# Kernel optimization log

Measured on AMD Instinct MI355X. Metric: run time of the kernel, lower is better.

## Reference

```python
import jax, jax.numpy as jnp
import numpy as np

EPS = 1e-5

def _bn_eval(x, gamma, beta, mean, var):
    return (x - mean) * (gamma / jnp.sqrt(var + EPS)) + beta

def setup_inputs() -> dict:
    key = jax.random.key(0)
    ks = jax.random.split(key, 12)
    N, E, D, C, H = 100000, 1000000, 64, 32, 128
    fused = 4 * D + C  # 288
    z = jax.random.normal(ks[0], (N, D), dtype=jnp.float32)
    edge_index = jax.random.randint(ks[1], (2, E), 0, N, dtype=jnp.int64)
    edge_context = jax.random.normal(ks[2], (E, C), dtype=jnp.float32)
    W1 = jax.random.normal(ks[3], (fused, H), dtype=jnp.float32) / np.sqrt(fused)
    b1 = jnp.zeros((H,), jnp.float32)
    g1 = jnp.ones((H,), jnp.float32); be1 = jnp.zeros((H,), jnp.float32)
    m1 = jnp.zeros((H,), jnp.float32); v1 = jnp.ones((H,), jnp.float32)
    W2 = jax.random.normal(ks[4], (H, H // 2), dtype=jnp.float32) / np.sqrt(H)
    b2 = jnp.zeros((H // 2,), jnp.float32)
    g2 = jnp.ones((H // 2,), jnp.float32); be2 = jnp.zeros((H // 2,), jnp.float32)
    m2 = jnp.zeros((H // 2,), jnp.float32); v2 = jnp.ones((H // 2,), jnp.float32)
    W3 = jax.random.normal(ks[5], (H // 2, 1), dtype=jnp.float32) / np.sqrt(H // 2)
    b3 = jnp.zeros((1,), jnp.float32)
    return {"z": z, "edge_index": edge_index, "edge_context": edge_context,
            "W1": W1, "b1": b1, "g1": g1, "be1": be1, "m1": m1, "v1": v1,
            "W2": W2, "b2": b2, "g2": g2, "be2": be2, "m2": m2, "v2": v2,
            "W3": W3, "b3": b3}

def reference(z, edge_index, edge_context,
              W1, b1, g1, be1, m1, v1,
              W2, b2, g2, be2, m2, v2,
              W3, b3):
    # gather endpoint embeddings: [E, D]
    src = z[edge_index[0]]
    dst = z[edge_index[1]]
    # fused features: [E, 4*D + C]
    fused = jnp.concatenate([src, dst, src * dst, jnp.abs(src - dst), edge_context], axis=1)
    x = jax.nn.relu(_bn_eval(fused @ W1 + b1, g1, be1, m1, v1))
    x = jax.nn.relu(_bn_eval(x @ W2 + b2, g2, be2, m2, v2))
    return (x @ W3 + b3).reshape(-1)
```

## Files before the change

kernel.cpp:

```cpp
#include <hip/hip_runtime.h>
#include <hip/hip_bf16.h>

typedef __attribute__((ext_vector_type(8))) short bf16x8;
typedef __attribute__((ext_vector_type(4))) float f32x4;
typedef __attribute__((ext_vector_type(4))) unsigned int u32x4;
typedef __attribute__((ext_vector_type(2))) unsigned int u32x2;
typedef __attribute__((ext_vector_type(2))) __bf16 bf16x2v;

#define EPS 1e-5f

__device__ inline unsigned short f2bf(float x) {
  unsigned int u = __builtin_bit_cast(unsigned int, x);
  unsigned int r = (u + 0x7FFFu + ((u >> 16) & 1u)) >> 16;
  return (unsigned short)r;
}

__device__ inline unsigned int cvtpk(float a, float b) {
  bf16x2v v = {(__bf16)a, (__bf16)b};
  return __builtin_bit_cast(unsigned int, v);
}

#define MFMA16(A, B, C) __builtin_amdgcn_mfma_f32_16x16x32_bf16((A), (B), (C), 0, 0, 0)

__global__ void prep_kernel(const float* __restrict__ W1, const float* __restrict__ W2,
                            const float* __restrict__ b1, const float* __restrict__ g1,
                            const float* __restrict__ be1, const float* __restrict__ m1,
                            const float* __restrict__ v1,
                            const float* __restrict__ b2, const float* __restrict__ g2,
                            const float* __restrict__ be2, const float* __restrict__ m2,
                            const float* __restrict__ v2,
                            unsigned short* __restrict__ w1f, unsigned short* __restrict__ w2f,
                            float* __restrict__ sc) {
  int t = blockIdx.x * 256 + threadIdx.x;
  if (t < 36864) {
    int j = t & 7, l = (t >> 3) & 63, f = t >> 9;
    int kb = f >> 3, nb = f & 7;
    int rk = kb * 32 + ((l >> 4) << 3) + j;
    int cn = (nb << 4) + (l & 15);
    w1f[t] = f2bf(W1[rk * 128 + cn]);
  } else if (t < 45056) {
    int o = t - 36864;
    int j = o & 7, l = (o >> 3) & 63, f = o >> 9;
    int kb = f >> 2, nb = f & 3;
    int s = kb * 32 + ((l >> 4) << 3) + j;
    int rk = (s & 96) | ((s & 1) << 4) | ((s >> 1) & 15);
    int cn = (nb << 4) + (l & 15);
    w2f[o] = f2bf(W2[rk * 64 + cn]);
  } else if (t < 45184) {
    int j = t - 45056;
    float s = g1[j] * rsqrtf(v1[j] + EPS);
    sc[j] = s;
    sc[128 + j] = (b1[j] - m1[j]) * s + be1[j];
  } else if (t < 45248) {
    int j = t - 45184;
    float s = g2[j] * rsqrtf(v2[j] + EPS);
    sc[256 + j] = s;
    sc[320 + j] = (b2[j] - m2[j]) * s + be2[j];
  }
}

#define F_SC_OFF 73728
#define F_A_OFF 75776
#define F_L3_OFF 157696
#define F_LDS_TOTAL 158720

#define WRITE_A_F()                                                                              \
  do {                                                                                           \
    const int rswz_ = (sr & 7) << 4;                                                             \
    char* rowp_ = AR + sr * 640;                                                                 \
    u32x4 ps_ = {cvtpk(sv0[0], sv0[1]), cvtpk(sv0[2], sv0[3]), cvtpk(sv1[0], sv1[1]),            \
                 cvtpk(sv1[2], sv1[3])};                                                         \
    u32x4 pd_ = {cvtpk(dv0[0], dv0[1]), cvtpk(dv0[2], dv0[3]), cvtpk(dv1[0], dv1[1]),            \
                 cvtpk(dv1[2], dv1[3])};                                                         \
    u32x4 pp_ = {cvtpk(sv0[0] * dv0[0], sv0[1] * dv0[1]), cvtpk(sv0[2] * dv0[2], sv0[3] * dv0[3]),\
                 cvtpk(sv1[0] * dv1[0], sv1[1] * dv1[1]), cvtpk(sv1[2] * dv1[2], sv1[3] * dv1[3])};\
    u32x4 pa_ = {cvtpk(fabsf(sv0[0] - dv0[0]), fabsf(sv0[1] - dv0[1])),                          \
                 cvtpk(fabsf(sv0[2] - dv0[2]), fabsf(sv0[3] - dv0[3])),                          \
                 cvtpk(fabsf(sv1[0] - dv1[0]), fabsf(sv1[1] - dv1[1])),                          \
                 cvtpk(fabsf(sv1[2] - dv1[2]), fabsf(sv1[3] - dv1[3]))};                         \
    u32x2 pc_ = {cvtpk(cv[0], cv[1]), cvtpk(cv[2], cv[3])};                                      \
    *(u32x4*)(rowp_ + ((sh * 16) ^ rswz_)) = ps_;                                                \
    *(u32x4*)(rowp_ + ((128 + sh * 16) ^ rswz_)) = pd_;                                          \
    *(u32x4*)(rowp_ + ((256 + sh * 16) ^ rswz_)) = pp_;                                          \
    *(u32x4*)(rowp_ + ((384 + sh * 16) ^ rswz_)) = pa_;                                          \
    *(u32x2*)(rowp_ + 512 + ((sh * 8) ^ rswz_)) = pc_;                                           \
  } while (0)

#define GATHER_NEXT_F(tg)                                                                        \
  do {                                                                                           \
    const f32x4* zs_ = (const f32x4*)(z + ((size_t)i0n * 64 + sh * 8));                          \
    sv0 = zs_[0];                                                                                \
    sv1 = zs_[1];                                                                                \
    const f32x4* zd_ = (const f32x4*)(z + ((size_t)i1n * 64 + sh * 8));                          \
    dv0 = zd_[0];                                                                                \
    dv1 = zd_[1];                                                                                \
    int eg_ = ((tg) << 7) + sr;                                                                  \
    int esg_ = eg_ < E ? eg_ : E - 1;                                                            \
    cv = *(const f32x4*)(ctx + (size_t)esg_ * 32 + sh * 4);                                      \
    int tn_ = (tg) + grid;                                                                       \
    if (tn_ >= nblk) tn_ = (tg);                                                                 \
    int en_ = (tn_ << 7) + sr;                                                                   \
    int esn_ = en_ < E ? en_ : E - 1;                                                            \
    i0n = ei[esn_];                                                                              \
    i1n = ei[E + esn_];                                                                          \
  } while (0)

__global__ __launch_bounds__(1024, 4) void fused_kernel_f(
    const float* __restrict__ z, const int* __restrict__ ei, const float* __restrict__ ctx,
    const unsigned short* __restrict__ w1f, const unsigned short* __restrict__ w2f,
    const float* __restrict__ sc, const float* __restrict__ w3, const float* __restrict__ b3,
    float* __restrict__ out, int E, int nblk) {
  extern __shared__ char lds[];
  char* W1L = lds;
  float* SC = (float*)(lds + F_SC_OFF);
  char* AR = lds + F_A_OFF;
  char* X1 = lds + F_A_OFF;
  float* l3 = (float*)(lds + F_L3_OFF);

  const int tid = threadIdx.x;
  const int lane = tid & 63, wave = tid >> 6;
  const int g = lane >> 4, lq = lane & 15;
  const int wr = wave >> 2, wc = wave & 3;
  const int w2r = wave >> 1, w2c = wave & 1;
  const int sr = tid >> 3, sh = tid & 7;
  const int grid = gridDim.x;

  {
    const f32x4* s = (const f32x4*)w1f;
    f32x4* d = (f32x4*)W1L;
#pragma unroll
    for (int i = 0; i < 4; i++) d[i * 1024 + tid] = s[i * 1024 + tid];
    if (tid < 512) d[4096 + tid] = s[4096 + tid];
    if (tid < 128) {
      SC[tid] = sc[tid];
      SC[128 + tid] = sc[128 + tid];
    } else if (tid < 192) {
      int j = tid - 128;
      SC[256 + j] = sc[256 + j];
      SC[320 + j] = sc[320 + j];
      SC[384 + j] = w3[j];
    } else if (tid == 192) {
      SC[448] = b3[0];
    }
  }

  bf16x8 w2g0, w2g1, w2g2, w2g3, w2h0, w2h1, w2h2, w2h3;
  {
    const bf16x8* W2G = (const bf16x8*)w2f;
    w2g0 = W2G[(0 * 4 + w2c * 2 + 0) * 64 + lane];
    w2h0 = W2G[(0 * 4 + w2c * 2 + 1) * 64 + lane];
    w2g1 = W2G[(1 * 4 + w2c * 2 + 0) * 64 + lane];
    w2h1 = W2G[(1 * 4 + w2c * 2 + 1) * 64 + lane];
    w2g2 = W2G[(2 * 4 + w2c * 2 + 0) * 64 + lane];
    w2h2 = W2G[(2 * 4 + w2c * 2 + 1) * 64 + lane];
    w2g3 = W2G[(3 * 4 + w2c * 2 + 0) * 64 + lane];
    w2h3 = W2G[(3 * 4 + w2c * 2 + 1) * 64 + lane];
  }

  f32x4 sv0, sv1, dv0, dv1, cv;
  int i0n, i1n;
  int t = blockIdx.x;

  {
    int e = (t << 7) + sr;
    int es = e < E ? e : E - 1;
    int a0 = ei[es], a1 = ei[E + es];
    cv = *(const f32x4*)(ctx + (size_t)es * 32 + sh * 4);
    const f32x4* zs = (const f32x4*)(z + ((size_t)a0 * 64 + sh * 8));
    sv0 = zs[0];
    sv1 = zs[1];
    const f32x4* zd = (const f32x4*)(z + ((size_t)a1 * 64 + sh * 8));
    dv0 = zd[0];
    dv1 = zd[1];
    int tn = t + grid;
    if (tn >= nblk) tn = t;
    int en = (tn << 7) + sr;
    int esn = en < E ? en : E - 1;
    i0n = ei[esn];
    i1n = ei[E + esn];
  }
  WRITE_A_F();
  {
    int tn = t + grid;
    if (tn >= nblk) tn = t;
    GATHER_NEXT_F(tn);
  }
  __syncthreads();

  for (; t < nblk; t += grid) {
    f32x4 acc00 = {0.f, 0.f, 0.f, 0.f}, acc01 = acc00, acc10 = acc00, acc11 = acc00;
    const bf16x8* W1F = (const bf16x8*)W1L;
    const int row0 = wr * 32 + lq, row1 = row0 + 16;
    const int swz0 = (row0 & 7) << 4, swz1 = (row1 & 7) << 4;
    const char* ap0 = AR + row0 * 640;
    const char* ap1 = AR + row1 * 640;
#pragma unroll
    for (int kb = 0; kb < 9; kb++) {
      bf16x8 a0 = *(const bf16x8*)(ap0 + ((kb * 64 + g * 16) ^ swz0));
      bf16x8 a1 = *(const bf16x8*)(ap1 + ((kb * 64 + g * 16) ^ swz1));
      bf16x8 b0 = W1F[(kb * 8 + wc * 2 + 0) * 64 + lane];
      bf16x8 b1 = W1F[(kb * 8 + wc * 2 + 1) * 64 + lane];
      acc00 = MFMA16(a0, b0, acc00);
      acc01 = MFMA16(a0, b1, acc01);
      acc10 = MFMA16(a1, b0, acc10);
      acc11 = MFMA16(a1, b1, acc11);
    }
    __syncthreads();

    {
      const int col0 = wc * 32 + lq;
      const float s1v0 = SC[col0], c1v0 = SC[128 + col0];
      const float s1v1 = SC[col0 + 16], c1v1 = SC[128 + col0 + 16];
      const int xoff = wc * 64 + lq * 4;
#pragma unroll
      for (int j = 0; j < 4; j++) {
        int rowa = wr * 32 + 4 * g + j;
        unsigned int pA = cvtpk(fmaxf(acc00[j] * s1v0 + c1v0, 0.f),
                                fmaxf(acc01[j] * s1v1 + c1v1, 0.f));
        *(unsigned int*)(X1 + rowa * 256 + (xoff ^ ((rowa & 7) << 4))) = pA;
        int rowb = rowa + 16;
        unsigned int pB = cvtpk(fmaxf(acc10[j] * s1v0 + c1v0, 0.f),
                                fmaxf(acc11[j] * s1v1 + c1v1, 0.f));
        *(unsigned int*)(X1 + rowb * 256 + (xoff ^ ((rowb & 7) << 4))) = pB;
      }
    }
    __syncthreads();

    f32x4 acc2A = {0.f, 0.f, 0.f, 0.f}, acc2B = acc2A;
    {
      const int row = w2r * 16 + lq;
      const int swz = (row & 7) << 4;
      const char* xp = X1 + row * 256;
      bf16x8 a0 = *(const bf16x8*)(xp + ((0 * 64 + g * 16) ^ swz));
      acc2A = MFMA16(a0, w2g0, acc2A);
      acc2B = MFMA16(a0, w2h0, acc2B);
      bf16x8 a1 = *(const bf16x8*)(xp + ((1 * 64 + g * 16) ^ swz));
      acc2A = MFMA16(a1, w2g1, acc2A);
      acc2B = MFMA16(a1, w2h1, acc2B);
      bf16x8 a2 = *(const bf16x8*)(xp + ((2 * 64 + g * 16) ^ swz));
      acc2A = MFMA16(a2, w2g2, acc2A);
      acc2B = MFMA16(a2, w2h2, acc2B);
      bf16x8 a3 = *(const bf16x8*)(xp + ((3 * 64 + g * 16) ^ swz));
      acc2A = MFMA16(a3, w2g3, acc2A);
      acc2B = MFMA16(a3, w2h3, acc2B);
    }

    const int colA = w2c * 32 + lq, colB = colA + 16;
    const float s2A = SC[256 + colA], c2A = SC[320 + colA];
    const float s2B = SC[256 + colB], c2B = SC[320 + colB];
    const float w3A = SC[384 + colA], w3B = SC[384 + colB];
#pragma unroll
    for (int j = 0; j < 4; j++) {
      float vA = fmaxf(acc2A[j] * s2A + c2A, 0.f);
      float vB = fmaxf(acc2B[j] * s2B + c2B, 0.f);
      float p = vA * w3A + vB * w3B;
      p += __shfl_xor(p, 1);
      p += __shfl_xor(p, 2);
      p += __shfl_xor(p, 4);
      p += __shfl_xor(p, 8);
      if (lq == 0) l3[(w2r * 16 + 4 * g + j) * 2 + w2c] = p;
    }
    __syncthreads();

    WRITE_A_F();
    {
      int tn2 = t + 2 * grid;
      if (tn2 >= nblk) tn2 = t + grid < nblk ? t + grid : t;
      GATHER_NEXT_F(tn2);
    }
    if (tid < 128) {
      int e = (t << 7) + tid;
      if (e < E) out[e] = l3[tid * 2] + l3[tid * 2 + 1] + SC[448];
    }
    __syncthreads();
  }
}

extern "C" void kernel_launch(void* const* d_in, const int* in_sizes, int n_in,
                              void* d_out, int out_size, void* d_ws, size_t ws_size,
                              hipStream_t stream) {
  const float* z = (const float*)d_in[0];
  const int* ei = (const int*)d_in[1];
  const float* ctx = (const float*)d_in[2];
  const float* W1 = (const float*)d_in[3];
  const float* b1 = (const float*)d_in[4];
  const float* g1 = (const float*)d_in[5];
  const float* be1 = (const float*)d_in[6];
  const float* m1 = (const float*)d_in[7];
  const float* v1 = (const float*)d_in[8];
  const float* W2 = (const float*)d_in[9];
  const float* b2 = (const float*)d_in[10];
  const float* g2 = (const float*)d_in[11];
  const float* be2 = (const float*)d_in[12];
  const float* m2 = (const float*)d_in[13];
  const float* v2 = (const float*)d_in[14];
  const float* W3 = (const float*)d_in[15];
  const float* b3 = (const float*)d_in[16];
  float* out = (float*)d_out;
  const int E = out_size;

  unsigned short* w1f = (unsigned short*)d_ws;
  unsigned short* w2f = (unsigned short*)((char*)d_ws + 73728);
  float* sc = (float*)((char*)d_ws + 90112);

  prep_kernel<<<177, 256, 0, stream>>>(W1, W2, b1, g1, be1, m1, v1,
                                       b2, g2, be2, m2, v2, w1f, w2f, sc);

  const int nblk = (E + 127) >> 7;
  (void)hipFuncSetAttribute((const void*)fused_kernel_f,
                            hipFuncAttributeMaxDynamicSharedMemorySize, F_LDS_TOTAL);
  fused_kernel_f<<<256, 1024, F_LDS_TOTAL, stream>>>(z, ei, ctx, w1f, w2f, sc, W3, b3,
                                                     out, E, nblk);
}
```

Before: 137.1 us.

## Derive product and abs-diff features from bf16 src/dst in registers instead of LDS

Adds a variant fused kernel whose LDS A tile holds only src, dst and context (384 bytes per row instead of 640). The src*dst and |src-dst| MFMA operands are recomputed in registers from the bf16 fragments already loaded for the src/dst MFMAs. This cuts LDS writes, reads and footprint but adds per-wave VALU work inside the layer-1 loop. The products are now formed from bf16-rounded inputs, which changes numerics slightly. The host falls back to the old kernel if the new one spills to scratch.

```diff
diff --git a/kernel.cpp b/kernel.cpp
--- a/kernel.cpp
+++ b/kernel.cpp
@@ -21,6 +21,23 @@
 }
 
 #define MFMA16(A, B, C) __builtin_amdgcn_mfma_f32_16x16x32_bf16((A), (B), (C), 0, 0, 0)
+
+__device__ inline void derive_pa(bf16x8 s, bf16x8 d, bf16x8* pr, bf16x8* ad) {
+  u32x4 su = __builtin_bit_cast(u32x4, s);
+  u32x4 du = __builtin_bit_cast(u32x4, d);
+  u32x4 pu, au;
+#pragma unroll
+  for (int i = 0; i < 4; i++) {
+    float slo = __builtin_bit_cast(float, su[i] << 16);
+    float shi = __builtin_bit_cast(float, su[i] & 0xFFFF0000u);
+    float dlo = __builtin_bit_cast(float, du[i] << 16);
+    float dhi = __builtin_bit_cast(float, du[i] & 0xFFFF0000u);
+    pu[i] = cvtpk(slo * dlo, shi * dhi);
+    au[i] = cvtpk(fabsf(slo - dlo), fabsf(shi - dhi));
+  }
+  *pr = __builtin_bit_cast(bf16x8, pu);
+  *ad = __builtin_bit_cast(bf16x8, au);
+}
 
 __global__ void prep_kernel(const float* __restrict__ W1, const float* __restrict__ W2,
                             const float* __restrict__ b1, const float* __restrict__ g1,
@@ -59,6 +76,243 @@
   }
 }
 
+#define V_SC_OFF 73728
+#define V_A_OFF 75776
+#define V_L3_OFF 124928
+#define V_LDS_TOTAL 125952
+
+#define WRITE_A_V()                                                                              \
+  do {                                                                                           \
+    const int rswz_ = (sr & 7) << 4;                                                             \
+    char* rowp_ = AV + sr * 384;                                                                 \
+    u32x4 ps_ = {cvtpk(sv0[0], sv0[1]), cvtpk(sv0[2], sv0[3]), cvtpk(sv1[0], sv1[1]),            \
+                 cvtpk(sv1[2], sv1[3])};                                                         \
+    u32x4 pd_ = {cvtpk(dv0[0], dv0[1]), cvtpk(dv0[2], dv0[3]), cvtpk(dv1[0], dv1[1]),            \
+                 cvtpk(dv1[2], dv1[3])};                                                         \
+    u32x2 pc_ = {cvtpk(cv[0], cv[1]), cvtpk(cv[2], cv[3])};                                      \
+    *(u32x4*)(rowp_ + ((sh * 16) ^ rswz_)) = ps_;                                                \
+    *(u32x4*)(rowp_ + ((128 + sh * 16) ^ rswz_)) = pd_;                                          \
+    *(u32x2*)(rowp_ + ((256 + sh * 8) ^ rswz_)) = pc_;                                           \
+  } while (0)
+
+#define GATHER_NEXT_V(tg)                                                                        \
+  do {                                                                                           \
+    const f32x4* zs_ = (const f32x4*)(z + ((size_t)i0n * 64 + sh * 8));                          \
+    sv0 = zs_[0];                                                                                \
+    sv1 = zs_[1];                                                                                \
+    const f32x4* zd_ = (const f32x4*)(z + ((size_t)i1n * 64 + sh * 8));                          \
+    dv0 = zd_[0];                                                                                \
+    dv1 = zd_[1];                                                                                \
+    int eg_ = ((tg) << 7) + sr;                                                                  \
+    int esg_ = eg_ < E ? eg_ : E - 1;                                                            \
+    cv = *(const f32x4*)(ctx + (size_t)esg_ * 32 + sh * 4);                                      \
+    int tn_ = (tg) + grid;                                                                       \
+    if (tn_ >= nblk) tn_ = (tg);                                                                 \
+    int en_ = (tn_ << 7) + sr;                                                                   \
+    int esn_ = en_ < E ? en_ : E - 1;                                                            \
+    i0n = ei[esn_];                                                                              \
+    i1n = ei[E + esn_];                                                                          \
+  } while (0)
+
+#define L1PAIR_V(KS)                                                                             \
+  do {                                                                                           \
+    bf16x8 s0_ = *(const bf16x8*)(ap0 + (((KS) * 64 + g * 16) ^ swz0));                          \
+    bf16x8 s1_ = *(const bf16x8*)(ap1 + (((KS) * 64 + g * 16) ^ swz0));                          \
+    bf16x8 d0_ = *(const bf16x8*)(ap0 + ((128 + (KS) * 64 + g * 16) ^ swz0));                    \
+    bf16x8 d1_ = *(const bf16x8*)(ap1 + ((128 + (KS) * 64 + g * 16) ^ swz0));                    \
+    bf16x8 b0_ = W1F[((KS) * 8 + wc * 2 + 0) * 64 + lane];                                       \
+    bf16x8 b1_ = W1F[((KS) * 8 + wc * 2 + 1) * 64 + lane];                                       \
+    acc00 = MFMA16(s0_, b0_, acc00); acc01 = MFMA16(s0_, b1_, acc01);                            \
+    acc10 = MFMA16(s1_, b0_, acc10); acc11 = MFMA16(s1_, b1_, acc11);                            \
+    b0_ = W1F[(((KS) + 2) * 8 + wc * 2 + 0) * 64 + lane];                                        \
+    b1_ = W1F[(((KS) + 2) * 8 + wc * 2 + 1) * 64 + lane];                                        \
+    acc00 = MFMA16(d0_, b0_, acc00); acc01 = MFMA16(d0_, b1_, acc01);                            \
+    acc10 = MFMA16(d1_, b0_, acc10); acc11 = MFMA16(d1_, b1_, acc11);                            \
+    bf16x8 p0_, a0_, p1_, a1_;                                                                   \
+    derive_pa(s0_, d0_, &p0_, &a0_);                                                             \
+    derive_pa(s1_, d1_, &p1_, &a1_);                                                             \
+    b0_ = W1F[(((KS) + 4) * 8 + wc * 2 + 0) * 64 + lane];                                        \
+    b1_ = W1F[(((KS) + 4) * 8 + wc * 2 + 1) * 64 + lane];                                        \
+    acc00 = MFMA16(p0_, b0_, acc00); acc01 = MFMA16(p0_, b1_, acc01);                            \
+    acc10 = MFMA16(p1_, b0_, acc10); acc11 = MFMA16(p1_, b1_, acc11);                            \
+    b0_ = W1F[(((KS) + 6) * 8 + wc * 2 + 0) * 64 + lane];                                        \
+    b1_ = W1F[(((KS) + 6) * 8 + wc * 2 + 1) * 64 + lane];                                        \
+    acc00 = MFMA16(a0_, b0_, acc00); acc01 = MFMA16(a0_, b1_, acc01);                            \
+    acc10 = MFMA16(a1_, b0_, acc10); acc11 = MFMA16(a1_, b1_, acc11);                            \
+  } while (0)
+
+__global__ __launch_bounds__(1024) void fused_kernel_v(
+    const float* __restrict__ z, const int* __restrict__ ei, const float* __restrict__ ctx,
+    const unsigned short* __restrict__ w1f, const unsigned short* __restrict__ w2f,
+    const float* __restrict__ sc, const float* __restrict__ w3, const float* __restrict__ b3,
+    float* __restrict__ out, int E, int nblk) {
+  extern __shared__ char lds[];
+  char* W1L = lds;
+  float* SC = (float*)(lds + V_SC_OFF);
+  char* AV = lds + V_A_OFF;
+  char* X1 = lds + V_A_OFF;
+  float* l3 = (float*)(lds + V_L3_OFF);
+
+  const int tid = threadIdx.x;
+  const int lane = tid & 63, wave = tid >> 6;
+  const int g = lane >> 4, lq = lane & 15;
+  const int wr = wave >> 2, wc = wave & 3;
+  const int w2r = wave >> 1, w2c = wave & 1;
+  const int sr = tid >> 3, sh = tid & 7;
+  const int grid = gridDim.x;
+
+  {
+    const f32x4* s = (const f32x4*)w1f;
+    f32x4* d = (f32x4*)W1L;
+#pragma unroll
+    for (int i = 0; i < 4; i++) d[i * 1024 + tid] = s[i * 1024 + tid];
+    if (tid < 512) d[4096 + tid] = s[4096 + tid];
+    if (tid < 128) {
+      SC[tid] = sc[tid];
+      SC[128 + tid] = sc[128 + tid];
+    } else if (tid < 192) {
+      int j = tid - 128;
+      SC[256 + j] = sc[256 + j];
+      SC[320 + j] = sc[320 + j];
+      SC[384 + j] = w3[j];
+    } else if (tid == 192) {
+      SC[448] = b3[0];
+    }
+  }
+
+  bf16x8 w2g0, w2g1, w2g2, w2g3, w2h0, w2h1, w2h2, w2h3;
+  {
+    const bf16x8* W2G = (const bf16x8*)w2f;
+    w2g0 = W2G[(0 * 4 + w2c * 2 + 0) * 64 + lane];
+    w2h0 = W2G[(0 * 4 + w2c * 2 + 1) * 64 + lane];
+    w2g1 = W2G[(1 * 4 + w2c * 2 + 0) * 64 + lane];
+    w2h1 = W2G[(1 * 4 + w2c * 2 + 1) * 64 + lane];
+    w2g2 = W2G[(2 * 4 + w2c * 2 + 0) * 64 + lane];
+    w2h2 = W2G[(2 * 4 + w2c * 2 + 1) * 64 + lane];
+    w2g3 = W2G[(3 * 4 + w2c * 2 + 0) * 64 + lane];
+    w2h3 = W2G[(3 * 4 + w2c * 2 + 1) * 64 + lane];
+  }
+
+  f32x4 sv0, sv1, dv0, dv1, cv;
+  int i0n, i1n;
+  int t = blockIdx.x;
+
+  {
+    int e = (t << 7) + sr;
+    int es = e < E ? e : E - 1;
+    int a0 = ei[es], a1 = ei[E + es];
+    cv = *(const f32x4*)(ctx + (size_t)es * 32 + sh * 4);
+    const f32x4* zs = (const f32x4*)(z + ((size_t)a0 * 64 + sh * 8));
+    sv0 = zs[0];
+    sv1 = zs[1];
+    const f32x4* zd = (const f32x4*)(z + ((size_t)a1 * 64 + sh * 8));
+    dv0 = zd[0];
+    dv1 = zd[1];
+    int tn = t + grid;
+    if (tn >= nblk) tn = t;
+    int en = (tn << 7) + sr;
+    int esn = en < E ? en : E - 1;
+    i0n = ei[esn];
+    i1n = ei[E + esn];
+  }
+  WRITE_A_V();
+  {
+    int tn = t + grid;
+    if (tn >= nblk) tn = t;
+    GATHER_NEXT_V(tn);
+  }
+  __syncthreads();
+
+  const bf16x8* W1F = (const bf16x8*)W1L;
+  for (; t < nblk; t += grid) {
+    f32x4 acc00 = {0.f, 0.f, 0.f, 0.f}, acc01 = acc00, acc10 = acc00, acc11 = acc00;
+    const int row0 = wr * 32 + lq;
+    const int swz0 = (row0 & 7) << 4;
+    const char* ap0 = AV + row0 * 384;
+    const char* ap1 = ap0 + 16 * 384;
+    L1PAIR_V(0);
+    L1PAIR_V(1);
+    {
+      bf16x8 c0 = *(const bf16x8*)(ap0 + ((256 + g * 16) ^ swz0));
+      bf16x8 c1 = *(const bf16x8*)(ap1 + ((256 + g * 16) ^ swz0));
+      bf16x8 b0 = W1F[(8 * 8 + wc * 2 + 0) * 64 + lane];
+      bf16x8 b1 = W1F[(8 * 8 + wc * 2 + 1) * 64 + lane];
+      acc00 = MFMA16(c0, b0, acc00);
+      acc01 = MFMA16(c0, b1, acc01);
+      acc10 = MFMA16(c1, b0, acc10);
+      acc11 = MFMA16(c1, b1, acc11);
+    }
+    __syncthreads();
+
+    {
+      const int col0 = wc * 32 + lq;
+      const float s1v0 = SC[col0], c1v0 = SC[128 + col0];
+      const float s1v1 = SC[col0 + 16], c1v1 = SC[128 + col0 + 16];
+      const int xoff = wc * 64 + lq * 4;
+#pragma unroll
+      for (int j = 0; j < 4; j++) {
+        int rowa = wr * 32 + 4 * g + j;
+        unsigned int pA = cvtpk(fmaxf(acc00[j] * s1v0 + c1v0, 0.f),
+                                fmaxf(acc01[j] * s1v1 + c1v1, 0.f));
+        *(unsigned int*)(X1 + rowa * 256 + (xoff ^ ((rowa & 7) << 4))) = pA;
+        int rowb = rowa + 16;
+        unsigned int pB = cvtpk(fmaxf(acc10[j] * s1v0 + c1v0, 0.f),
+                                fmaxf(acc11[j] * s1v1 + c1v1, 0.f));
+        *(unsigned int*)(X1 + rowb * 256 + (xoff ^ ((rowb & 7) << 4))) = pB;
+      }
+    }
+    __syncthreads();
+
+    f32x4 acc2A = {0.f, 0.f, 0.f, 0.f}, acc2B = acc2A;
+    {
+      const int row = w2r * 16 + lq;
+      const int swz = (row & 7) << 4;
+      const char* xp = X1 + row * 256;
+      bf16x8 a0 = *(const bf16x8*)(xp + ((0 * 64 + g * 16) ^ swz));
+      acc2A = MFMA16(a0, w2g0, acc2A);
+      acc2B = MFMA16(a0, w2h0, acc2B);
+      bf16x8 a1 = *(const bf16x8*)(xp + ((1 * 64 + g * 16) ^ swz));
+      acc2A = MFMA16(a1, w2g1, acc2A);
+      acc2B = MFMA16(a1, w2h1, acc2B);
+      bf16x8 a2 = *(const bf16x8*)(xp + ((2 * 64 + g * 16) ^ swz));
+      acc2A = MFMA16(a2, w2g2, acc2A);
+      acc2B = MFMA16(a2, w2h2, acc2B);
+      bf16x8 a3 = *(const bf16x8*)(xp + ((3 * 64 + g * 16) ^ swz));
+      acc2A = MFMA16(a3, w2g3, acc2A);
+      acc2B = MFMA16(a3, w2h3, acc2B);
+    }
+
+    const int colA = w2c * 32 + lq, colB = colA + 16;
+    const float s2A = SC[256 + colA], c2A = SC[320 + colA];
+    const float s2B = SC[256 + colB], c2B = SC[320 + colB];
+    const float w3A = SC[384 + colA], w3B = SC[384 + colB];
+#pragma unroll
+    for (int j = 0; j < 4; j++) {
+      float vA = fmaxf(acc2A[j] * s2A + c2A, 0.f);
+      float vB = fmaxf(acc2B[j] * s2B + c2B, 0.f);
+      float p = vA * w3A + vB * w3B;
+      p += __shfl_xor(p, 1);
+      p += __shfl_xor(p, 2);
+      p += __shfl_xor(p, 4);
+      p += __shfl_xor(p, 8);
+      if (lq == 0) l3[(w2r * 16 + 4 * g + j) * 2 + w2c] = p;
+    }
+    __syncthreads();
+
+    WRITE_A_V();
+    {
+      int tn2 = t + 2 * grid;
+      if (tn2 >= nblk) tn2 = t + grid < nblk ? t + grid : t;
+      GATHER_NEXT_V(tn2);
+    }
+    if (tid < 128) {
+      int e = (t << 7) + tid;
+      if (e < E) out[e] = l3[tid * 2] + l3[tid * 2 + 1] + SC[448];
+    }
+    __syncthreads();
+  }
+}
+
 #define F_SC_OFF 73728
 #define F_A_OFF 75776
 #define F_L3_OFF 157696
@@ -307,8 +561,22 @@
                                        b2, g2, be2, m2, v2, w1f, w2f, sc);
 
   const int nblk = (E + 127) >> 7;
-  (void)hipFuncSetAttribute((const void*)fused_kernel_f,
-                            hipFuncAttributeMaxDynamicSharedMemorySize, F_LDS_TOTAL);
-  fused_kernel_f<<<256, 1024, F_LDS_TOTAL, stream>>>(z, ei, ctx, w1f, w2f, sc, W3, b3,
-                                                     out, E, nblk);
-}
+
+  hipFuncAttributes attr;
+  bool use_v = false;
+  if (hipFuncGetAttributes(&attr, (const void*)fused_kernel_v) == hipSuccess) {
+    use_v = (attr.localSizeBytes < 16);
+  }
+
+  if (use_v) {
+    (void)hipFuncSetAttribute((const void*)fused_kernel_v,
+                              hipFuncAttributeMaxDynamicSharedMemorySize, V_LDS_TOTAL);
+    fused_kernel_v<<<256, 1024, V_LDS_TOTAL, stream>>>(z, ei, ctx, w1f, w2f, sc, W3, b3,
+                                                       out, E, nblk);
+  } else {
+    (void)hipFuncSetAttribute((const void*)fused_kernel_f,
+                              hipFuncAttributeMaxDynamicSharedMemorySize, F_LDS_TOTAL);
+    fused_kernel_f<<<256, 1024, F_LDS_TOTAL, stream>>>(z, ei, ctx, w1f, w2f, sc, W3, b3,
+                                                       out, E, nblk);
+  }
+}
```

After: 136.6 us. No clear change (-0.4%).
